# Kernel tuning notes

Measured on AMD Instinct MI355X. Metric: run time of the kernel, lower is better.

Reference implementation:

```python
import jax, jax.numpy as jnp
import numpy as np
from jax import lax

B, C, H, W = 32, 3, 384, 384
BN_EPS = 1e-5


def setup_inputs() -> dict:
    key = jax.random.key(0)
    ks = jax.random.split(key, 18)
    s = 0.05
    inp = {
        "x": jax.random.normal(ks[0], (B, C, H, W), jnp.float32),
        # stand-in rgb branch head: global-avg-pool(3) -> Linear(3,2)
        "w_rgb": jax.random.normal(ks[1], (3, 2), jnp.float32) * s,
        "b_rgb": jnp.zeros((2,), jnp.float32),
        # freq_conv params
        "conv1_w": jax.random.normal(ks[2], (64, 3, 7, 7), jnp.float32) * s,
        "conv1_b": jnp.zeros((64,), jnp.float32),
        "bn1_g": jnp.ones((64,), jnp.float32),
        "bn1_b": jnp.zeros((64,), jnp.float32),
        "conv2_w": jax.random.normal(ks[3], (128, 64, 3, 3), jnp.float32) * s,
        "conv2_b": jnp.zeros((128,), jnp.float32),
        "bn2_g": jnp.ones((128,), jnp.float32),
        "bn2_b": jnp.zeros((128,), jnp.float32),
        # fusion MLP: 130 -> 256 -> 128 -> 2 (weights stored (in,out))
        "fc1_w": jax.random.normal(ks[4], (130, 256), jnp.float32) * s,
        "fc1_b": jnp.zeros((256,), jnp.float32),
        "fc2_w": jax.random.normal(ks[5], (256, 128), jnp.float32) * s,
        "fc2_b": jnp.zeros((128,), jnp.float32),
        "fc3_w": jax.random.normal(ks[6], (128, 2), jnp.float32) * s,
        "fc3_b": jnp.zeros((2,), jnp.float32),
    }
    return inp


def _conv(x, w, b, stride, pad):
    y = lax.conv_general_dilated(
        x, w, window_strides=(stride, stride),
        padding=((pad, pad), (pad, pad)),
        dimension_numbers=("NCHW", "OIHW", "NCHW"))
    return y + b[None, :, None, None]


def _bn_eval(x, g, b):
    # eval-mode BatchNorm with running_mean=0, running_var=1
    scale = g / jnp.sqrt(1.0 + BN_EPS)
    return x * scale[None, :, None, None] + b[None, :, None, None]


def _maxpool3s2p1(x):
    return lax.reduce_window(
        x, -jnp.inf, lax.max, (1, 1, 3, 3), (1, 1, 2, 2),
        padding=((0, 0), (0, 0), (1, 1), (1, 1)))


def _freq_features(x):
    # batched replacement of the per-sample/per-channel numpy FFT loop
    f = jnp.fft.fftshift(jnp.fft.fft2(x, axes=(-2, -1)), axes=(-2, -1))
    mag = jnp.log(jnp.abs(f) + 1.0)
    mean = mag.mean(axis=(-2, -1), keepdims=True)
    std = mag.std(axis=(-2, -1), keepdims=True)
    return (mag - mean) / (std + 1e-8)


def reference(x, w_rgb, b_rgb, conv1_w, conv1_b, bn1_g, bn1_b,
              conv2_w, conv2_b, bn2_g, bn2_b,
              fc1_w, fc1_b, fc2_w, fc2_b, fc3_w, fc3_b):
    # rgb branch (stand-in for external EfficientNet detector): GAP -> Linear(3,2)
    rgb_out = x.mean(axis=(2, 3)) @ w_rgb + b_rgb  # (B,2)

    freq = _freq_features(x)  # (B,3,H,W)
    h = jax.nn.relu(_bn_eval(_conv(freq, conv1_w, conv1_b, 2, 3), bn1_g, bn1_b))
    h = _maxpool3s2p1(h)
    h = jax.nn.relu(_bn_eval(_conv(h, conv2_w, conv2_b, 1, 1), bn2_g, bn2_b))
    freq_out = h.mean(axis=(2, 3))  # AdaptiveAvgPool2d((1,1)) -> (B,128)

    z = jnp.concatenate([rgb_out, freq_out], axis=1)  # (B,130)
    z = jax.nn.relu(z @ fc1_w + fc1_b)
    z = jax.nn.relu(z @ fc2_w + fc2_b)
    return z @ fc3_w + fc3_b  # (B,2)
```

## Files before the change

kernel.cpp:

```cpp
#include <hip/hip_runtime.h>
#include <math.h>

#define NB    32
#define NC    3
#define NIMG  (NB*NC)
#define NS    384
#define HWSZ  (NS*NS)
#define C1OUT 64
#define C1DIM 192
#define PDIM  96
#define PHW   (PDIM*PDIM)
#define C2OUT 128
#define KWH   200
#define BHW   192
#define PI_F  3.14159265358979323846f

static const size_t OFF_T    = 0;
static const size_t OFF_TW1  = 8192;
static const size_t OFF_TW2H = 32768;
static const size_t OFF_B    = 1179648;
static const size_t OFF_C0   = 1179648 + 28311552;
static const size_t OFF_P    = 29638656;
static const size_t OFF_S    = 57802752;
static const size_t OFF_SM_F = 133300224;
static const size_t OFF_SM_C = 76677120;
static const size_t NEED_F   = 133318912;

#define WI(i) ((i) + ((i) >> 4))

typedef __attribute__((ext_vector_type(8))) short bf16x8_t;
typedef __attribute__((ext_vector_type(4))) float f32x4_t;
union U16 { unsigned u[4]; uint4 q; bf16x8_t v; };

__device__ __forceinline__ float wave_sum(float v){
  #pragma unroll
  for (int off = 32; off; off >>= 1) v += __shfl_down(v, off);
  return v;
}
__device__ __forceinline__ unsigned short f2bf(float f){
  unsigned u = __float_as_uint(f);
  u += 0x7FFFu + ((u >> 16) & 1u);
  return (unsigned short)(u >> 16);
}
__device__ __forceinline__ float bf2f(unsigned short h){
  return __uint_as_float(((unsigned)h) << 16);
}
__device__ __forceinline__ unsigned pmax16(unsigned a, unsigned b){
  unsigned al = a & 0xffffu, ah = a >> 16, bl = b & 0xffffu, bh = b >> 16;
  unsigned ml = al > bl ? al : bl, mh = ah > bh ? ah : bh;
  return (mh << 16) | ml;
}
__device__ __forceinline__ uint4 pmax8(uint4 a, uint4 b){
  uint4 r;
  r.x = pmax16(a.x, b.x); r.y = pmax16(a.y, b.y);
  r.z = pmax16(a.z, b.z); r.w = pmax16(a.w, b.w);
  return r;
}
__device__ __forceinline__ int mod384(int v){ return v >= NS ? v - NS : v; }
__device__ __forceinline__ float2 cmul(float2 a, float2 b){
  return make_float2(a.x*b.x - a.y*b.y, a.x*b.y + a.y*b.x);
}

__global__ void k_prep(const float* __restrict__ w1, const float* __restrict__ w2,
    float2* __restrict__ T, unsigned short* __restrict__ w1p,
    unsigned short* __restrict__ w2ph){
  int idx = blockIdx.x*256 + (int)threadIdx.x;
  if (idx < NS){
    float ang = -2.0f*PI_F*(float)idx/(float)NS;
    T[NS + idx] = make_float2(cosf(ang), sinf(ang));
  }
  if (idx < 64*192){
    int oc = idx / 192, k = idx - oc*192;
    int rk = k >> 3, kw = k & 7;
    float val = 0.f;
    if (rk < 21 && kw < 7){
      int ic = rk / 7, kh = rk - 7*ic;
      val = w1[oc*147 + ic*49 + kh*7 + kw];
    }
    w1p[idx] = f2bf(val);
  }
  if (idx < 128*576){
    int oc = idx / 576, k = idx - oc*576;
    int tap = k >> 6, ic = k & 63;
    w2ph[idx] = f2bf(w2[(size_t)oc*576 + ic*9 + tap]);
  }
}

__global__ __launch_bounds__(192) void k_dft_rows(const float* __restrict__ x,
    const float2* __restrict__ T, float2* __restrict__ A,
    float* __restrict__ rgbsum, int bc0){
  __shared__ float2 work[4][408];
  __shared__ float rs[3];
  const float2* Trow = T + NS;
  int blk = blockIdx.x;
  int bcl = blk / 48, rg = blk % 48;
  int bc = bc0 + bcl;
  int t = threadIdx.x;
  const float* xp = x + (size_t)bc*HWSZ + (size_t)rg*8*NS;
  int nA = t,        rA = nA % 3, iA = (rA*128) + (__brev((unsigned)(nA/3)) >> 25);
  int nB = t + 192,  rB = nB % 3, iB = (rB*128) + (__brev((unsigned)(nB/3)) >> 25);
  float lsum = 0.f;
  #pragma unroll
  for (int c = 0; c < 4; ++c){
    float a0 = xp[(2*c)*NS + nA],   b0 = xp[(2*c+1)*NS + nA];
    float a1 = xp[(2*c)*NS + nB],   b1 = xp[(2*c+1)*NS + nB];
    work[c][WI(iA)] = make_float2(a0, b0);
    work[c][WI(iB)] = make_float2(a1, b1);
    lsum += a0 + b0 + a1 + b1;
  }
  float ws = wave_sum(lsum);
  if ((t & 63) == 0) rs[t >> 6] = ws;
  __syncthreads();
  if (t == 0) atomicAdd(&rgbsum[bc], rs[0] + rs[1] + rs[2]);

  int sub = t >> 6, j = t & 63;
  #pragma unroll
  for (int st = 0; st < 7; ++st){
    int half = 1 << st;
    int pos = j & (half - 1);
    int ia = sub*128 + (((j >> st) << (st + 1)) | pos);
    int ib = ia + half;
    float2 tw = Trow[(192 >> st) * pos];
    #pragma unroll
    for (int c = 0; c < 4; ++c){
      float2 a = work[c][WI(ia)], b = cmul(work[c][WI(ib)], tw);
      work[c][WI(ia)] = make_float2(a.x + b.x, a.y + b.y);
      work[c][WI(ib)] = make_float2(a.x - b.x, a.y - b.y);
    }
    __syncthreads();
  }
  int k1a = t & 127, k1b = (t + 192) & 127;
  float2 w1 = Trow[t], w2 = Trow[(2*t) % 384];
  float2 Xa[4], Xb[4];
  #pragma unroll
  for (int c = 0; c < 4; ++c){
    float2 p1 = cmul(w1, work[c][WI(128 + k1a)]);
    float2 p2 = cmul(w2, work[c][WI(256 + k1a)]);
    float2 y0 = work[c][WI(k1a)];
    Xa[c] = make_float2(y0.x + p1.x + p2.x, y0.y + p1.y + p2.y);
    float2 q1 = cmul(w1, work[c][WI(128 + k1b)]);
    float2 q2 = cmul(w2, work[c][WI(256 + k1b)]);
    float2 z0 = work[c][WI(k1b)];
    Xb[c] = make_float2(z0.x - q1.x + q2.x, z0.y - q1.y + q2.y);
  }
  __syncthreads();
  #pragma unroll
  for (int c = 0; c < 4; ++c){ work[c][WI(t)] = Xa[c]; work[c][WI(t + 192)] = Xb[c]; }
  __syncthreads();
  int tm = (t == 0) ? 0 : (384 - t);
  #pragma unroll
  for (int c = 0; c < 4; ++c){
    float2 Zk = Xa[c];
    float2 Zm = work[c][WI(tm)];
    size_t b0r = ((size_t)bcl*NS + rg*8 + 2*c)*KWH;
    size_t b1r = b0r + KWH;
    A[b0r + t] = make_float2(0.5f*(Zk.x + Zm.x), 0.5f*(Zk.y - Zm.y));
    A[b1r + t] = make_float2(0.5f*(Zk.y + Zm.y), 0.5f*(Zm.x - Zk.x));
    if (t == 0){
      float2 Zn = Xb[c];
      A[b0r + 192] = make_float2(Zn.x, 0.f);
      A[b1r + 192] = make_float2(Zn.y, 0.f);
    }
  }
}

__global__ __launch_bounds__(192) void k_dft_cols(const float2* __restrict__ A,
    const float2* __restrict__ T, float* __restrict__ Bh, float* __restrict__ col0,
    float* __restrict__ stats, int bc0){
  __shared__ float2 work[8][408];
  __shared__ float rs[6];
  float* mgp = (float*)work;
  const float2* Trow = T + NS;
  int blk = blockIdx.x;
  int bcl = blk / 25, cg = blk % 25;
  int bc = bc0 + bcl;
  int kw0 = cg*8;
  int cols = (cg == 24) ? 1 : 8;
  int t = threadIdx.x;
  const float2* Al = A + (size_t)bcl*NS*KWH;
  if (cols == 8){
    #pragma unroll
    for (int i = 0; i < 16; ++i){
      int lin = i*192 + t;
      int h = lin >> 3, c = lin & 7;
      int r = h % 3;
      work[c][WI(r*128 + (__brev((unsigned)(h/3)) >> 25))] = Al[(size_t)h*KWH + kw0 + c];
    }
  } else {
    for (int h = t; h < NS; h += 192){
      int r = h % 3;
      work[0][WI(r*128 + (__brev((unsigned)(h/3)) >> 25))] = Al[(size_t)h*KWH + kw0];
    }
  }
  __syncthreads();
  int sub = t >> 6, j = t & 63;
  #pragma unroll
  for (int st = 0; st < 7; ++st){
    int half = 1 << st;
    int pos = j & (half - 1);
    int ia = sub*128 + (((j >> st) << (st + 1)) | pos);
    int ib = ia + half;
    float2 tw = Trow[(192 >> st) * pos];
    #pragma unroll
    for (int c = 0; c < 8; ++c){
      if (c < cols){
        float2 a = work[c][WI(ia)], b = cmul(work[c][WI(ib)], tw);
        work[c][WI(ia)] = make_float2(a.x + b.x, a.y + b.y);
        work[c][WI(ib)] = make_float2(a.x - b.x, a.y - b.y);
      }
    }
    __syncthreads();
  }
  int k1a = t & 127, k1b = (t + 192) & 127;
  float2 w1 = Trow[t], w2 = Trow[(2*t) % 384];
  float s1 = 0.f, s2 = 0.f;
  float ma[8], mb[8];
  #pragma unroll
  for (int c = 0; c < 8; ++c){
    ma[c] = 0.f; mb[c] = 0.f;
    if (c < cols){
      float2 p1 = cmul(w1, work[c][WI(128 + k1a)]);
      float2 p2 = cmul(w2, work[c][WI(256 + k1a)]);
      float2 y0 = work[c][WI(k1a)];
      float2 Xa = make_float2(y0.x + p1.x + p2.x, y0.y + p1.y + p2.y);
      float2 q1 = cmul(w1, work[c][WI(128 + k1b)]);
      float2 q2 = cmul(w2, work[c][WI(256 + k1b)]);
      float2 z0 = work[c][WI(k1b)];
      float2 Xb = make_float2(z0.x - q1.x + q2.x, z0.y - q1.y + q2.y);
      ma[c] = logf(sqrtf(Xa.x*Xa.x + Xa.y*Xa.y) + 1.f);
      mb[c] = logf(sqrtf(Xb.x*Xb.x + Xb.y*Xb.y) + 1.f);
      int kw = kw0 + c;
      float wgt = (kw >= 1 && kw <= 191) ? 2.f : 1.f;
      s1 += wgt*(ma[c] + mb[c]);
      s2 += wgt*(ma[c]*ma[c] + mb[c]*mb[c]);
    }
  }
  __syncthreads();
  #pragma unroll
  for (int c = 0; c < 8; ++c){
    if (c < cols){
      mgp[(t + 192)*9 + c] = ma[c];
      mgp[t*9 + c]         = mb[c];
    }
  }
  __syncthreads();
  if (cols == 8){
    float* Bhc = Bh + (size_t)bc*NS*BHW;
    #pragma unroll
    for (int rr = 0; rr < 2; ++rr){
      int u = t + rr*192;
      float* row = Bhc + (size_t)u*BHW + kw0;
      *(float4*)(row)     = make_float4(mgp[u*9+0], mgp[u*9+1], mgp[u*9+2], mgp[u*9+3]);
      *(float4*)(row + 4) = make_float4(mgp[u*9+4], mgp[u*9+5], mgp[u*9+6], mgp[u*9+7]);
    }
  } else {
    float* c0c = col0 + (size_t)bc*NS;
    #pragma unroll
    for (int rr = 0; rr < 2; ++rr){
      int u = t + rr*192;
      c0c[u] = mgp[u*9];
    }
  }
  float w1s = wave_sum(s1), w2s = wave_sum(s2);
  if ((t & 63) == 0){ rs[t >> 6] = w1s; rs[3 + (t >> 6)] = w2s; }
  __syncthreads();
  if (t == 0){
    atomicAdd(&stats[bc*2],     rs[0] + rs[1] + rs[2]);
    atomicAdd(&stats[bc*2 + 1], rs[3] + rs[4] + rs[5]);
  }
}

__global__ void k_finalize(const float* __restrict__ stats, const float* __restrict__ rgbsum,
                           float* __restrict__ ss, float* __restrict__ rgbmean){
  int t = threadIdx.x;
  if (t < NIMG){
    const float inv_n = 1.f / 147456.f;
    float mean = stats[t*2] * inv_n;
    float var  = fmaxf(stats[t*2 + 1] * inv_n - mean*mean, 0.f);
    float inv  = 1.f / (sqrtf(var) + 1e-8f);
    ss[t*2]     = inv;
    ss[t*2 + 1] = -mean * inv;
    rgbmean[t]  = rgbsum[t] * inv_n;
  }
}

__global__ __launch_bounds__(256) void k_conv1mfma(const float* __restrict__ Bh,
    const float* __restrict__ col0, const float* __restrict__ ss,
    const unsigned short* __restrict__ w1p, const float* __restrict__ b1,
    const float* __restrict__ g1, const float* __restrict__ bb1,
    unsigned short* __restrict__ E, int b0){
  __shared__ unsigned short pt[3*37*40];
  int blk = blockIdx.x;
  int li = blk / 144, rem = blk - li*144;
  int rg = rem / 12, cg = rem - rg*12;
  int r0 = rg*16, c0 = cg*16;
  int b = b0 + li;
  int t = threadIdx.x;
  float sc[3], sh[3];
  #pragma unroll
  for (int ic = 0; ic < 3; ++ic){ sc[ic] = ss[(b*3 + ic)*2]; sh[ic] = ss[(b*3 + ic)*2 + 1]; }
  const int h0 = 2*r0 - 3, w0 = 2*c0 - 3;
  for (int lin = t; lin < 3*37*40; lin += 256){
    int ic = lin / 1480; int r = lin - ic*1480;
    int hr = r / 40, wc = r - hr*40;
    int hg = h0 + hr, wg = w0 + wc;
    bool v = (wc < 38) && ((unsigned)hg < (unsigned)NS) && ((unsigned)wg < (unsigned)NS);
    float raw = 0.f;
    if (v){
      const float* Bc = Bh + (size_t)(b*3 + ic)*NS*BHW;
      if (wg >= 192)      raw = Bc[(size_t)hg*BHW + (wg - 192)];
      else if (wg >= 1)   raw = Bc[(size_t)mod384(NS - hg)*BHW + (192 - wg)];
      else                raw = col0[(size_t)(b*3 + ic)*NS + hg];
    }
    pt[lin] = v ? f2bf(fmaf(raw, sc[ic], sh[ic])) : (unsigned short)0;
  }
  __syncthreads();

  int wave = t >> 6, lane = t & 63;
  int lm = lane & 15, lg = lane >> 4;
  U16 bf[6];
  #pragma unroll
  for (int ks = 0; ks < 6; ++ks)
    bf[ks].q = *(const uint4*)(w1p + (wave*16 + lm)*192 + ks*32 + lg*8);
  int cbase[6];
  #pragma unroll
  for (int ks = 0; ks < 6; ++ks){
    int rk = ks*4 + lg;
    if (rk > 20) rk = 20;
    int ic = rk / 7, kh = rk - 7*ic;
    cbase[ks] = ic*1480 + kh*40 + 2*lm;
  }
  const float bneps = rsqrtf(1.f + 1e-5f);
  float4 b4  = *(const float4*)(b1  + wave*16 + lg*4);
  float4 g4  = *(const float4*)(g1  + wave*16 + lg*4);
  float4 bb4 = *(const float4*)(bb1 + wave*16 + lg*4);
  float4 gs4 = make_float4(g4.x*bneps, g4.y*bneps, g4.z*bneps, g4.w*bneps);
  unsigned short* Eb = E + (((size_t)li*C1DIM + r0)*C1DIM + c0 + lm)*64 + wave*16 + lg*4;

  #pragma unroll 1
  for (int rt = 0; rt < 16; ++rt){
    f32x4_t acc = {b4.x, b4.y, b4.z, b4.w};
    #pragma unroll
    for (int ks = 0; ks < 6; ++ks){
      U16 a;
      const unsigned* pp = (const unsigned*)&pt[cbase[ks] + 80*rt];
      a.u[0] = pp[0]; a.u[1] = pp[1]; a.u[2] = pp[2]; a.u[3] = pp[3];
      acc = __builtin_amdgcn_mfma_f32_16x16x32_bf16(bf[ks].v, a.v, acc, 0, 0, 0);
    }
    ushort4 o;
    o.x = f2bf(fmaxf(fmaf(acc[0], gs4.x, bb4.x), 0.f));
    o.y = f2bf(fmaxf(fmaf(acc[1], gs4.y, bb4.y), 0.f));
    o.z = f2bf(fmaxf(fmaf(acc[2], gs4.z, bb4.z), 0.f));
    o.w = f2bf(fmaxf(fmaf(acc[3], gs4.w, bb4.w), 0.f));
    *(ushort4*)(Eb + (size_t)rt*C1DIM*64) = o;
  }
}

__global__ __launch_bounds__(256) void k_pool(const unsigned short* __restrict__ E,
    unsigned short* __restrict__ P){
  int lin = blockIdx.x*256 + (int)threadIdx.x;
  int g = lin & 7; int rm = lin >> 3;
  int pw = rm % PDIM; int rm2 = rm / PDIM;
  int ph = rm2 % PDIM; int li = rm2 / PDIM;
  const unsigned short* Eb = E + (size_t)li*C1DIM*C1DIM*64 + g*8;
  uint4 mx = make_uint4(0u,0u,0u,0u);
  #pragma unroll
  for (int dh = 0; dh < 3; ++dh){
    int eh = 2*ph - 1 + dh;
    if ((unsigned)eh >= (unsigned)C1DIM) continue;
    #pragma unroll
    for (int dw = 0; dw < 3; ++dw){
      int ew = 2*pw - 1 + dw;
      if ((unsigned)ew >= (unsigned)C1DIM) continue;
      mx = pmax8(mx, *(const uint4*)(Eb + ((size_t)eh*C1DIM + ew)*64));
    }
  }
  *(uint4*)(P + ((size_t)rm)*64 + g*8) = mx;
}

__global__ __launch_bounds__(512) void k_conv2mfma(const unsigned short* __restrict__ P,
    const unsigned short* __restrict__ w2ph,
    const float* __restrict__ b2, const float* __restrict__ g2,
    const float* __restrict__ bb2, float* __restrict__ freq_acc, int b0){
  __shared__ unsigned short sD[10*1152];
  int blk = blockIdx.x;
  int li = blk / 72, tile = blk - li*72;
  int rb = tile / 6, cb = tile - rb*6;
  int r0 = rb*8, c0 = cb*16;
  int b = b0 + li;
  int t = threadIdx.x;
  const unsigned short* Pb = P + (size_t)li*PHW*64;
  for (int lin = t; lin < 1440; lin += 512){
    int g = lin & 7; int rm = lin >> 3;
    int wp = rm % 18, hp = rm / 18;
    int ph = r0 + hp - 1, pw = c0 + wp - 1;
    uint4 v = make_uint4(0u,0u,0u,0u);
    if ((unsigned)ph < (unsigned)PDIM && (unsigned)pw < (unsigned)PDIM)
      v = *(const uint4*)(Pb + ((size_t)ph*PDIM + pw)*64 + g*8);
    *(uint4*)&sD[hp*1152 + g*144 + wp*8] = v;
  }
  __syncthreads();

  int wave = t >> 6, lane = t & 63;
  int lm = lane & 15, lg = lane >> 4;
  int octile = wave*16;
  const float bneps = rsqrtf(1.f + 1e-5f);
  float4 b4  = *(const float4*)(b2  + octile + lg*4);
  float4 g4  = *(const float4*)(g2  + octile + lg*4);
  float4 bb4 = *(const float4*)(bb2 + octile + lg*4);
  f32x4_t acc[8];
  #pragma unroll
  for (int nt = 0; nt < 8; ++nt){
    acc[nt][0] = b4.x; acc[nt][1] = b4.y; acc[nt][2] = b4.z; acc[nt][3] = b4.w;
  }
  const unsigned short* whp = w2ph + (size_t)(octile + lm)*576;
  __builtin_amdgcn_s_setprio(1);
  #pragma unroll
  for (int ks = 0; ks < 18; ++ks){
    const int tap = ks >> 1, h32 = ks & 1;
    const int dh = tap / 3, dw = tap - 3*(tap/3);
    U16 wh;
    wh.q = *(const uint4*)(whp + ks*32 + lg*8);
    int base = (h32*4 + lg)*144 + (lm + dw)*8;
    #pragma unroll
    for (int nt = 0; nt < 8; ++nt){
      U16 a;
      a.q = *(const uint4*)&sD[(nt + dh)*1152 + base];
      acc[nt] = __builtin_amdgcn_mfma_f32_16x16x32_bf16(wh.v, a.v, acc[nt], 0, 0, 0);
    }
  }
  __builtin_amdgcn_s_setprio(0);
  float s0 = 0.f, s1 = 0.f, s2 = 0.f, s3 = 0.f;
  float gx = g4.x*bneps, gy = g4.y*bneps, gz = g4.z*bneps, gw = g4.w*bneps;
  #pragma unroll
  for (int nt = 0; nt < 8; ++nt){
    s0 += fmaxf(fmaf(acc[nt][0], gx, bb4.x), 0.f);
    s1 += fmaxf(fmaf(acc[nt][1], gy, bb4.y), 0.f);
    s2 += fmaxf(fmaf(acc[nt][2], gz, bb4.z), 0.f);
    s3 += fmaxf(fmaf(acc[nt][3], gw, bb4.w), 0.f);
  }
  #pragma unroll
  for (int off = 1; off < 16; off <<= 1){
    s0 += __shfl_xor(s0, off);
    s1 += __shfl_xor(s1, off);
    s2 += __shfl_xor(s2, off);
    s3 += __shfl_xor(s3, off);
  }
  if (lm == 0){
    float* fa = freq_acc + (size_t)b*C2OUT + octile + lg*4;
    atomicAdd(fa + 0, s0); atomicAdd(fa + 1, s1);
    atomicAdd(fa + 2, s2); atomicAdd(fa + 3, s3);
  }
}

__global__ __launch_bounds__(256) void k_mlp(const float* __restrict__ rgbmean,
    const float* __restrict__ freq_acc, const float* __restrict__ w_rgb,
    const float* __restrict__ b_rgb, const float* __restrict__ fc1w,
    const float* __restrict__ fc1b, const float* __restrict__ fc2w,
    const float* __restrict__ fc2b, const float* __restrict__ fc3w,
    const float* __restrict__ fc3b, float* __restrict__ out){
  __shared__ float z[130], z1[256], z2[128];
  int b = blockIdx.x, t = threadIdx.x;
  if (t < 2){
    float s = b_rgb[t];
    #pragma unroll
    for (int c = 0; c < 3; ++c) s += rgbmean[b*3 + c] * w_rgb[c*2 + t];
    z[t] = s;
  }
  if (t < 128) z[2 + t] = freq_acc[b*C2OUT + t] * (1.f/9216.f);
  __syncthreads();
  { float s = fc1b[t];
    for (int k = 0; k < 130; ++k) s = fmaf(z[k], fc1w[k*256 + t], s);
    z1[t] = fmaxf(s, 0.f); }
  __syncthreads();
  if (t < 128){
    float s = fc2b[t];
    for (int k = 0; k < 256; ++k) s = fmaf(z1[k], fc2w[k*128 + t], s);
    z2[t] = fmaxf(s, 0.f); }
  __syncthreads();
  if (t < 2){
    float s = fc3b[t];
    for (int k = 0; k < 128; ++k) s = fmaf(z2[k], fc3w[k*2 + t], s);
    out[b*2 + t] = s; }
}

extern "C" void kernel_launch(void* const* d_in, const int* in_sizes, int n_in,
                              void* d_out, int out_size, void* d_ws, size_t ws_size,
                              hipStream_t stream){
  const float* x     = (const float*)d_in[0];
  const float* w_rgb = (const float*)d_in[1];
  const float* b_rgb = (const float*)d_in[2];
  const float* w1    = (const float*)d_in[3];
  const float* b1    = (const float*)d_in[4];
  const float* g1    = (const float*)d_in[5];
  const float* bb1   = (const float*)d_in[6];
  const float* w2    = (const float*)d_in[7];
  const float* b2    = (const float*)d_in[8];
  const float* g2    = (const float*)d_in[9];
  const float* bb2   = (const float*)d_in[10];
  const float* fc1w  = (const float*)d_in[11];
  const float* fc1b  = (const float*)d_in[12];
  const float* fc2w  = (const float*)d_in[13];
  const float* fc2b  = (const float*)d_in[14];
  const float* fc3w  = (const float*)d_in[15];
  const float* fc3b  = (const float*)d_in[16];

  const bool full = (ws_size >= NEED_F);
  const int dftloop = full ? 1 : 4;
  const int dftCH   = full ? 96 : 24;
  const int cvloop  = full ? 2 : 16;
  const int cvB     = full ? 16 : 2;

  char* ws = (char*)d_ws;
  float2* T  = (float2*)(ws + OFF_T);
  unsigned short* w1p  = (unsigned short*)(ws + OFF_TW1);
  unsigned short* w2ph = (unsigned short*)(ws + OFF_TW2H);
  float*  Bh   = (float*)(ws + OFF_B);
  float*  col0 = (float*)(ws + OFF_C0);
  unsigned short* P = (unsigned short*)(ws + OFF_P);
  float2* A    = (float2*)(ws + OFF_S);
  unsigned short* E = (unsigned short*)(ws + OFF_S);
  float*  sm = (float*)(ws + (full ? OFF_SM_F : OFF_SM_C));
  float* rgbsum = sm;
  float* stats  = sm + 96;
  float* freqa  = sm + 288;
  float* rgbm   = sm + 4384;
  float* ssb    = sm + 4480;

  hipMemsetAsync(sm, 0, 4672*sizeof(float), stream);
  k_prep<<<288, 256, 0, stream>>>(w1, w2, T, w1p, w2ph);
  for (int c = 0; c < dftloop; ++c){
    k_dft_rows<<<dftCH*48, 192, 0, stream>>>(x, T, A, rgbsum, c*dftCH);
    k_dft_cols<<<dftCH*25, 192, 0, stream>>>(A, T, Bh, col0, stats, c*dftCH);
  }
  k_finalize<<<1, 128, 0, stream>>>(stats, rgbsum, ssb, rgbm);
  for (int c = 0; c < cvloop; ++c){
    k_conv1mfma<<<cvB*144, 256, 0, stream>>>(Bh, col0, ssb, w1p, b1, g1, bb1, E, c*cvB);
    k_pool<<<cvB*288, 256, 0, stream>>>(E, P);
    k_conv2mfma<<<cvB*72, 512, 0, stream>>>(P, w2ph, b2, g2, bb2, freqa, c*cvB);
  }
  k_mlp<<<NB, 256, 0, stream>>>(rgbm, freqa, w_rgb, b_rgb, fc1w, fc1b,
                                fc2w, fc2b, fc3w, fc3b, (float*)d_out);
}
```

Measured before the change: 344.5 us.

## Run radix-2 FFT stages in registers with wave shuffles instead of LDS

The 128-point radix-2 stages in the row and column DFT kernels now run with two points per lane in registers. Stage 0 is done in place and stages 1-6 exchange partners via __shfl_xor within the 64-lane wave, which removes the per-stage LDS round trips and __syncthreads barriers. The padded WI() shared-memory indexing is dropped, since LDS is now touched only at load and store points with float4 accesses. This costs extra shuffle instructions and higher register pressure, especially in the 8-column kernel.

```diff
diff --git a/kernel.cpp b/kernel.cpp
--- a/kernel.cpp
+++ b/kernel.cpp
@@ -26,8 +26,6 @@
 static const size_t OFF_SM_C = 76677120;
 static const size_t NEED_F   = 133318912;
 
-#define WI(i) ((i) + ((i) >> 4))
-
 typedef __attribute__((ext_vector_type(8))) short bf16x8_t;
 typedef __attribute__((ext_vector_type(4))) float f32x4_t;
 union U16 { unsigned u[4]; uint4 q; bf16x8_t v; };
@@ -59,6 +57,9 @@
 __device__ __forceinline__ int mod384(int v){ return v >= NS ? v - NS : v; }
 __device__ __forceinline__ float2 cmul(float2 a, float2 b){
   return make_float2(a.x*b.x - a.y*b.y, a.x*b.y + a.y*b.x);
+}
+__device__ __forceinline__ float2 shfl_xor_f2(float2 v, int m){
+  return make_float2(__shfl_xor(v.x, m), __shfl_xor(v.y, m));
 }
 
 __global__ void k_prep(const float* __restrict__ w1, const float* __restrict__ w2,
@@ -89,7 +90,7 @@
 __global__ __launch_bounds__(192) void k_dft_rows(const float* __restrict__ x,
     const float2* __restrict__ T, float2* __restrict__ A,
     float* __restrict__ rgbsum, int bc0){
-  __shared__ float2 work[4][408];
+  __shared__ float2 work[4][384];
   __shared__ float rs[3];
   const float2* Trow = T + NS;
   int blk = blockIdx.x;
@@ -104,8 +105,8 @@
   for (int c = 0; c < 4; ++c){
     float a0 = xp[(2*c)*NS + nA],   b0 = xp[(2*c+1)*NS + nA];
     float a1 = xp[(2*c)*NS + nB],   b1 = xp[(2*c+1)*NS + nB];
-    work[c][WI(iA)] = make_float2(a0, b0);
-    work[c][WI(iB)] = make_float2(a1, b1);
+    work[c][iA] = make_float2(a0, b0);
+    work[c][iB] = make_float2(a1, b1);
     lsum += a0 + b0 + a1 + b1;
   }
   float ws = wave_sum(lsum);
@@ -113,45 +114,70 @@
   __syncthreads();
   if (t == 0) atomicAdd(&rgbsum[bc], rs[0] + rs[1] + rs[2]);
 
-  int sub = t >> 6, j = t & 63;
-  #pragma unroll
-  for (int st = 0; st < 7; ++st){
-    int half = 1 << st;
-    int pos = j & (half - 1);
-    int ia = sub*128 + (((j >> st) << (st + 1)) | pos);
-    int ib = ia + half;
-    float2 tw = Trow[(192 >> st) * pos];
+  int sub = t >> 6, l = t & 63;
+  float2 z0[4], z1[4];
+  #pragma unroll
+  for (int c = 0; c < 4; ++c){
+    float4 zz = *(const float4*)&work[c][sub*128 + 2*l];
+    z0[c] = make_float2(zz.x, zz.y);
+    z1[c] = make_float2(zz.z, zz.w);
+  }
+  #pragma unroll
+  for (int c = 0; c < 4; ++c){
+    float2 a = z0[c];
+    z0[c] = make_float2(a.x + z1[c].x, a.y + z1[c].y);
+    z1[c] = make_float2(a.x - z1[c].x, a.y - z1[c].y);
+  }
+  #pragma unroll
+  for (int st = 1; st < 7; ++st){
+    int half = 1 << st, m = half >> 1, step = 192 >> st;
+    int pos0 = (2*l) & (half - 1);
+    float2 w0 = Trow[step*pos0];
+    float2 w1v = Trow[step*(pos0 + 1)];
+    bool hi = (l & m) != 0;
+    float s = hi ? -1.f : 1.f;
     #pragma unroll
     for (int c = 0; c < 4; ++c){
-      float2 a = work[c][WI(ia)], b = cmul(work[c][WI(ib)], tw);
-      work[c][WI(ia)] = make_float2(a.x + b.x, a.y + b.y);
-      work[c][WI(ib)] = make_float2(a.x - b.x, a.y - b.y);
-    }
-    __syncthreads();
-  }
+      float2 o0 = shfl_xor_f2(z0[c], m);
+      float2 o1 = shfl_xor_f2(z1[c], m);
+      float2 b0 = hi ? z0[c] : o0;
+      float2 a0 = hi ? o0 : z0[c];
+      float2 b1 = hi ? z1[c] : o1;
+      float2 a1 = hi ? o1 : z1[c];
+      float2 p0 = cmul(b0, w0);
+      float2 p1 = cmul(b1, w1v);
+      z0[c] = make_float2(fmaf(s, p0.x, a0.x), fmaf(s, p0.y, a0.y));
+      z1[c] = make_float2(fmaf(s, p1.x, a1.x), fmaf(s, p1.y, a1.y));
+    }
+  }
+  #pragma unroll
+  for (int c = 0; c < 4; ++c)
+    *(float4*)&work[c][sub*128 + 2*l] = make_float4(z0[c].x, z0[c].y, z1[c].x, z1[c].y);
+  __syncthreads();
+
   int k1a = t & 127, k1b = (t + 192) & 127;
   float2 w1 = Trow[t], w2 = Trow[(2*t) % 384];
   float2 Xa[4], Xb[4];
   #pragma unroll
   for (int c = 0; c < 4; ++c){
-    float2 p1 = cmul(w1, work[c][WI(128 + k1a)]);
-    float2 p2 = cmul(w2, work[c][WI(256 + k1a)]);
-    float2 y0 = work[c][WI(k1a)];
+    float2 p1 = cmul(w1, work[c][128 + k1a]);
+    float2 p2 = cmul(w2, work[c][256 + k1a]);
+    float2 y0 = work[c][k1a];
     Xa[c] = make_float2(y0.x + p1.x + p2.x, y0.y + p1.y + p2.y);
-    float2 q1 = cmul(w1, work[c][WI(128 + k1b)]);
-    float2 q2 = cmul(w2, work[c][WI(256 + k1b)]);
-    float2 z0 = work[c][WI(k1b)];
-    Xb[c] = make_float2(z0.x - q1.x + q2.x, z0.y - q1.y + q2.y);
-  }
-  __syncthreads();
-  #pragma unroll
-  for (int c = 0; c < 4; ++c){ work[c][WI(t)] = Xa[c]; work[c][WI(t + 192)] = Xb[c]; }
+    float2 q1 = cmul(w1, work[c][128 + k1b]);
+    float2 q2 = cmul(w2, work[c][256 + k1b]);
+    float2 z0v = work[c][k1b];
+    Xb[c] = make_float2(z0v.x - q1.x + q2.x, z0v.y - q1.y + q2.y);
+  }
+  __syncthreads();
+  #pragma unroll
+  for (int c = 0; c < 4; ++c){ work[c][t] = Xa[c]; work[c][t + 192] = Xb[c]; }
   __syncthreads();
   int tm = (t == 0) ? 0 : (384 - t);
   #pragma unroll
   for (int c = 0; c < 4; ++c){
     float2 Zk = Xa[c];
-    float2 Zm = work[c][WI(tm)];
+    float2 Zm = work[c][tm];
     size_t b0r = ((size_t)bcl*NS + rg*8 + 2*c)*KWH;
     size_t b1r = b0r + KWH;
     A[b0r + t] = make_float2(0.5f*(Zk.x + Zm.x), 0.5f*(Zk.y - Zm.y));
@@ -167,7 +193,7 @@
 __global__ __launch_bounds__(192) void k_dft_cols(const float2* __restrict__ A,
     const float2* __restrict__ T, float* __restrict__ Bh, float* __restrict__ col0,
     float* __restrict__ stats, int bc0){
-  __shared__ float2 work[8][408];
+  __shared__ float2 work[8][384];
   __shared__ float rs[6];
   float* mgp = (float*)work;
   const float2* Trow = T + NS;
@@ -184,33 +210,65 @@
       int lin = i*192 + t;
       int h = lin >> 3, c = lin & 7;
       int r = h % 3;
-      work[c][WI(r*128 + (__brev((unsigned)(h/3)) >> 25))] = Al[(size_t)h*KWH + kw0 + c];
+      work[c][r*128 + (__brev((unsigned)(h/3)) >> 25)] = Al[(size_t)h*KWH + kw0 + c];
     }
   } else {
     for (int h = t; h < NS; h += 192){
       int r = h % 3;
-      work[0][WI(r*128 + (__brev((unsigned)(h/3)) >> 25))] = Al[(size_t)h*KWH + kw0];
-    }
-  }
-  __syncthreads();
-  int sub = t >> 6, j = t & 63;
-  #pragma unroll
-  for (int st = 0; st < 7; ++st){
-    int half = 1 << st;
-    int pos = j & (half - 1);
-    int ia = sub*128 + (((j >> st) << (st + 1)) | pos);
-    int ib = ia + half;
-    float2 tw = Trow[(192 >> st) * pos];
+      work[0][r*128 + (__brev((unsigned)(h/3)) >> 25)] = Al[(size_t)h*KWH + kw0];
+    }
+  }
+  __syncthreads();
+
+  int sub = t >> 6, l = t & 63;
+  float2 z0[8], z1[8];
+  #pragma unroll
+  for (int c = 0; c < 8; ++c){
+    if (c < cols){
+      float4 zz = *(const float4*)&work[c][sub*128 + 2*l];
+      z0[c] = make_float2(zz.x, zz.y);
+      z1[c] = make_float2(zz.z, zz.w);
+    }
+  }
+  #pragma unroll
+  for (int c = 0; c < 8; ++c){
+    if (c < cols){
+      float2 a = z0[c];
+      z0[c] = make_float2(a.x + z1[c].x, a.y + z1[c].y);
+      z1[c] = make_float2(a.x - z1[c].x, a.y - z1[c].y);
+    }
+  }
+  #pragma unroll
+  for (int st = 1; st < 7; ++st){
+    int half = 1 << st, m = half >> 1, step = 192 >> st;
+    int pos0 = (2*l) & (half - 1);
+    float2 w0 = Trow[step*pos0];
+    float2 w1v = Trow[step*(pos0 + 1)];
+    bool hi = (l & m) != 0;
+    float s = hi ? -1.f : 1.f;
     #pragma unroll
     for (int c = 0; c < 8; ++c){
       if (c < cols){
-        float2 a = work[c][WI(ia)], b = cmul(work[c][WI(ib)], tw);
-        work[c][WI(ia)] = make_float2(a.x + b.x, a.y + b.y);
-        work[c][WI(ib)] = make_float2(a.x - b.x, a.y - b.y);
+        float2 o0 = shfl_xor_f2(z0[c], m);
+        float2 o1 = shfl_xor_f2(z1[c], m);
+        float2 b0 = hi ? z0[c] : o0;
+        float2 a0 = hi ? o0 : z0[c];
+        float2 b1 = hi ? z1[c] : o1;
+        float2 a1 = hi ? o1 : z1[c];
+        float2 p0 = cmul(b0, w0);
+        float2 p1 = cmul(b1, w1v);
+        z0[c] = make_float2(fmaf(s, p0.x, a0.x), fmaf(s, p0.y, a0.y));
+        z1[c] = make_float2(fmaf(s, p1.x, a1.x), fmaf(s, p1.y, a1.y));
       }
     }
-    __syncthreads();
-  }
+  }
+  #pragma unroll
+  for (int c = 0; c < 8; ++c){
+    if (c < cols)
+      *(float4*)&work[c][sub*128 + 2*l] = make_float4(z0[c].x, z0[c].y, z1[c].x, z1[c].y);
+  }
+  __syncthreads();
+
   int k1a = t & 127, k1b = (t + 192) & 127;
   float2 w1 = Trow[t], w2 = Trow[(2*t) % 384];
   float s1 = 0.f, s2 = 0.f;
@@ -219,14 +277,14 @@
   for (int c = 0; c < 8; ++c){
     ma[c] = 0.f; mb[c] = 0.f;
     if (c < cols){
-      float2 p1 = cmul(w1, work[c][WI(128 + k1a)]);
-      float2 p2 = cmul(w2, work[c][WI(256 + k1a)]);
-      float2 y0 = work[c][WI(k1a)];
+      float2 p1 = cmul(w1, work[c][128 + k1a]);
+      float2 p2 = cmul(w2, work[c][256 + k1a]);
+      float2 y0 = work[c][k1a];
       float2 Xa = make_float2(y0.x + p1.x + p2.x, y0.y + p1.y + p2.y);
-      float2 q1 = cmul(w1, work[c][WI(128 + k1b)]);
-      float2 q2 = cmul(w2, work[c][WI(256 + k1b)]);
-      float2 z0 = work[c][WI(k1b)];
-      float2 Xb = make_float2(z0.x - q1.x + q2.x, z0.y - q1.y + q2.y);
+      float2 q1 = cmul(w1, work[c][128 + k1b]);
+      float2 q2 = cmul(w2, work[c][256 + k1b]);
+      float2 z0v = work[c][k1b];
+      float2 Xb = make_float2(z0v.x - q1.x + q2.x, z0v.y - q1.y + q2.y);
       ma[c] = logf(sqrtf(Xa.x*Xa.x + Xa.y*Xa.y) + 1.f);
       mb[c] = logf(sqrtf(Xb.x*Xb.x + Xb.y*Xb.y) + 1.f);
       int kw = kw0 + c;
```

Measured after the change: 356.1 us. 1.03x slower.
